# Performance work log

Measured on AMD Instinct MI355X. Metric: run time of the kernel, lower is better.

Reference implementation:

```python
import jax, jax.numpy as jnp
import numpy as np

# ---- static hyperparameters (from init_kwargs) ----
O_CH = 256        # out_channels
C_IN = 128        # in_channels
K = 3             # kernel_size
M = 9             # ALSH appended dims (m); m/(K*K)=1 extra input channel for Q
NUM_HASHES = 5
TABLE_SIZE = 2048
R = 4.0           # LSH bucket width
U = 0.99          # norm scaling constant
PAD = 1


def _conv(x, w):
    # NCHW conv, stride 1, padding 1, dilation 1 (per init_kwargs)
    return jax.lax.conv_general_dilated(
        x, w, window_strides=(1, 1), padding=[(PAD, PAD), (PAD, PAD)],
        dimension_numbers=("NCHW", "OIHW", "NCHW"))


def setup_inputs() -> dict:
    key = jax.random.key(0)
    k1, k2, k3, k4, k5 = jax.random.split(key, 5)
    x = jax.random.normal(k1, (32, C_IN, 56, 56), dtype=jnp.float32)
    weight = jax.random.normal(k2, (O_CH, C_IN, K, K), dtype=jnp.float32) * 0.05
    bias = jax.random.normal(k3, (O_CH,), dtype=jnp.float32) * 0.01
    # one stable-distribution hash vector per hash; dim = K*K*C_IN + M = 1161
    a = jax.random.normal(k4, (NUM_HASHES, K * K * C_IN + M), dtype=jnp.float32)
    b_unit = jax.random.uniform(k5, (NUM_HASHES,), dtype=jnp.float32)  # b = b_unit * R
    return {"x": x, "weight": weight, "bias": bias, "a": a, "b_unit": b_unit}


def reference(x, weight, bias, a, b_unit):
    B, C, H, W = x.shape
    O = weight.shape[0]
    b = b_unit * R  # b ~ U(0, r)

    # ---- table build: hash every kernel row (P = append norm powers) ----
    flat = weight.reshape(O, -1)                                   # [O, C*K*K]
    denom = jnp.linalg.norm(flat, axis=1).max()
    wU = (U / denom) * flat                                        # all rows ||.|| <= U < 1
    norms = jnp.linalg.norm(wU, axis=1)                            # [O]
    powers = norms[:, None] ** (2.0 ** jnp.arange(1, M + 1))       # [O, M]: ||x||^2,...,||x||^(2^M)
    Pw = jnp.concatenate([wU, powers], axis=1)                     # [O, C*K*K + M]
    hv = jnp.floor((Pw @ a.T + b[None, :]) / R).astype(jnp.int32)  # [O, NUM_HASHES]
    kernel_bucket = jnp.abs(jnp.fmod(hv, TABLE_SIZE))              # bucket of each kernel per hash

    # ---- vote: Q appends m/(K*K) channels of 0.5, conv with hash vectors as kernels ----
    extra = M // (K * K)
    xQ = jnp.concatenate(
        [x, jnp.full((B, extra, H, W), 0.5, dtype=x.dtype)], axis=1)  # [B, C+extra, H, W]
    a_kernel = a.reshape(NUM_HASHES, C + extra, K, K)
    dotted = _conv(xQ, a_kernel)                                   # [B, NUM_HASHES, H', W']
    dotted = jnp.transpose(dotted, (1, 0, 2, 3)).reshape(NUM_HASHES, -1)
    votes = jnp.floor((dotted + b[:, None]) / R).astype(jnp.int32)
    votes = jnp.abs(jnp.fmod(votes, TABLE_SIZE))                   # [NUM_HASHES, N]

    # per-hash bucket histogram via offset bincount, then best bucket per hash
    offset = (votes + jnp.arange(NUM_HASHES, dtype=jnp.int32)[:, None] * TABLE_SIZE).reshape(-1)
    counts = jnp.bincount(offset, length=NUM_HASHES * TABLE_SIZE).reshape(NUM_HASHES, TABLE_SIZE)
    selected = jnp.argmax(counts, axis=1).astype(jnp.int32)        # [NUM_HASHES]

    # ---- active set: union over selected buckets of kernels hashed there (any hash) ----
    active = jnp.any(kernel_bucket[:, :, None] == selected[None, None, :], axis=(1, 2))  # [O]
    # fallback (source draws random rows if empty): use all kernels
    active = jnp.where(jnp.any(active), active, jnp.ones_like(active))
    n_active = active.sum().astype(x.dtype)

    # ---- conv with active subset (static-shape: mask inactive output channels) ----
    out = _conv(x, weight) + bias[None, :, None, None]             # [B, O, H', W']
    out = out * active.astype(out.dtype)[None, :, None, None]
    out = out * (jnp.asarray(O, out.dtype) / n_active)             # out /= (|rows|/O)
    return out
```

## Files before the change

kernel.cpp:

```cpp
#include <hip/hip_runtime.h>
#include <hip/hip_bf16.h>
#include <stdint.h>

typedef __attribute__((ext_vector_type(8))) short  short8;
typedef __attribute__((ext_vector_type(4))) float  f32x4;

#define C_IN  128
#define O_CH  256
#define NH    5
#define TSIZE 2048
#define HWDIM 56
#define NPIX  3136
#define MTOT  100352
#define KTOT  1152
#define ADIM  1161
#define PADW  58
#define PPIX  3364
#define NHC   8
#define LBINS 192

static __device__ __forceinline__ unsigned short f2bf(float f) {
  unsigned int u = __float_as_uint(f);
  return (unsigned short)((u + 0x7fffu + ((u >> 16) & 1u)) >> 16);
}

static __device__ __forceinline__ void gload16(const unsigned short* g, unsigned short* l) {
  __builtin_amdgcn_global_load_lds(
      (const __attribute__((address_space(1))) void*)g,
      (__attribute__((address_space(3))) void*)l, 16, 0, 0);
}

#define WAITV(n) asm volatile("s_waitcnt vmcnt(" #n ")" ::: "memory")
static __device__ __forceinline__ void barsync() {
  asm volatile("" ::: "memory");
  __builtin_amdgcn_s_barrier();
  __builtin_amdgcn_sched_barrier(0);
  asm volatile("" ::: "memory");
}

__global__ void k_norms(const float* __restrict__ w, double* __restrict__ ssbuf) {
  int o = blockIdx.x, t = threadIdx.x;
  double ss = 0.;
  for (int i = t; i < KTOT; i += 64) { double v = (double)w[o * KTOT + i]; ss += v * v; }
  #pragma unroll
  for (int off = 32; off > 0; off >>= 1) ss += __shfl_down(ss, off, 64);
  if (t == 0) ssbuf[o] = ss;
}

__global__ __launch_bounds__(256) void k_table(const float* __restrict__ w,
    const float* __restrict__ a, const float* __restrict__ b_unit,
    const double* __restrict__ ssbuf, int* __restrict__ kbucket) {
  int o = blockIdx.x, t = threadIdx.x;
  __shared__ double red[256];
  __shared__ double r6[6][256];
  red[t] = ssbuf[t];
  __syncthreads();
  for (int s = 128; s; s >>= 1) { if (t < s) red[t] = fmax(red[t], red[t + s]); __syncthreads(); }
  double scale = 0.99 / sqrt(red[0]);
  double pd0 = 0, pd1 = 0, pd2 = 0, pd3 = 0, pd4 = 0, ss2 = 0;
  for (int i = t; i < KTOT; i += 256) {
    double wv = scale * (double)w[o * KTOT + i];
    ss2 += wv * wv;
    pd0 += wv * (double)a[0 * ADIM + i];
    pd1 += wv * (double)a[1 * ADIM + i];
    pd2 += wv * (double)a[2 * ADIM + i];
    pd3 += wv * (double)a[3 * ADIM + i];
    pd4 += wv * (double)a[4 * ADIM + i];
  }
  r6[0][t] = ss2; r6[1][t] = pd0; r6[2][t] = pd1; r6[3][t] = pd2; r6[4][t] = pd3; r6[5][t] = pd4;
  __syncthreads();
  for (int s = 128; s; s >>= 1) {
    if (t < s) { for (int q = 0; q < 6; ++q) r6[q][t] += r6[q][t + s]; }
    __syncthreads();
  }
  if (t == 0) {
    double nrm = sqrt(r6[0][0]);
    double q = nrm;
    double dp[NH] = {0, 0, 0, 0, 0};
    for (int j = 0; j < 9; ++j) {
      q = q * q;
      #pragma unroll
      for (int h = 0; h < NH; ++h) dp[h] += q * (double)a[h * ADIM + KTOT + j];
    }
    #pragma unroll
    for (int h = 0; h < NH; ++h) {
      double tot = r6[1 + h][0] + dp[h] + (double)b_unit[h] * 4.0;
      int hv = (int)floor(tot * 0.25);
      int bk = hv % TSIZE; if (bk < 0) bk = -bk;
      kbucket[o * NH + h] = bk;
    }
  }
}

__global__ __launch_bounds__(256) void k_prep(const float* __restrict__ w,
    const float* __restrict__ a, unsigned short* __restrict__ wpk,
    unsigned short* __restrict__ xpq, float* __restrict__ apk,
    int* __restrict__ ghist, int doPack, int qstride) {
  int bid = blockIdx.x, t = threadIdx.x;
  if (bid < 1152) {
    if (!doPack) return;
    int idx = bid * 256 + t;
    int kt = idx >> 13; int rem = idx & 8191;
    int o = rem >> 5; int cl = rem & 31;
    int kyx = kt >> 2, cq = kt & 3;
    wpk[idx] = f2bf(w[o * KTOT + (cq * 32 + cl) * 9 + kyx]);
  } else if (bid < 1175) {
    int i = (bid - 1152) * 256 + t;
    if (i < C_IN * 45) {
      int c = i / 45, r = i - c * 45;
      int h = r / 9, k = r - h * 9;
      apk[c * 48 + r] = a[h * ADIM + c * 9 + k];
    }
  } else if (bid < 1215) {
    int i = (bid - 1175) * 2048 + t;
    #pragma unroll
    for (int j = 0; j < 8; ++j) ghist[i + j * 256] = 0;
  } else {
    if (!doPack) return;
    int b2 = bid - 1215;
    int cq = b2 & 3; int rest = b2 >> 2;
    int r = rest % PADW, bl = rest / PADW;
    unsigned short* row = xpq + ((size_t)cq * qstride + (size_t)bl * PPIX + (size_t)r * PADW) * 32;
    if (r == 0 || r == PADW - 1) {
      for (int i = t; i < PADW * 32; i += 256) row[i] = 0;
    } else {
      if (t < 32) row[t] = 0;
      else if (t < 64) row[57 * 32 + (t - 32)] = 0;
    }
  }
}

__global__ __launch_bounds__(256) void k_vote3a(const float* __restrict__ x,
    const float* __restrict__ apk, float* __restrict__ pdot) {
  int g = blockIdx.y;
  int t = threadIdx.x;
  int p0 = blockIdx.x * 512 + t * 2;
  int bb = p0 / NPIX; int rem = p0 - bb * NPIX;
  int y = rem / HWDIM; int xxL = rem - y * HWDIM;
  bool xm = xxL > 0, xp = xxL < HWDIM - 2;
  bool y0 = y > 0, y2 = y < HWDIM - 1;
  const float* xb = x + ((size_t)bb * C_IN + g * 32) * NPIX + y * HWDIM + xxL;
  const float* ap = apk + (g * 32) * 48;
  float aL[NH] = {0, 0, 0, 0, 0}, aR[NH] = {0, 0, 0, 0, 0};
  for (int c = 0; c < 32; ++c) {
    const float* xc = xb + c * NPIX;
    float t0m = 0, t00 = 0, t01 = 0, t02 = 0;
    float m0m = 0, m02 = 0;
    float b0m = 0, b00 = 0, b01 = 0, b02 = 0;
    float m00 = xc[0], m01 = xc[1];
    if (xm) m0m = xc[-1];
    if (xp) m02 = xc[2];
    if (y0) { t00 = xc[-HWDIM]; t01 = xc[-HWDIM + 1]; if (xm) t0m = xc[-HWDIM - 1]; if (xp) t02 = xc[-HWDIM + 2]; }
    if (y2) { b00 = xc[HWDIM];  b01 = xc[HWDIM + 1];  if (xm) b0m = xc[HWDIM - 1];  if (xp) b02 = xc[HWDIM + 2]; }
    const float* ac = ap + c * 48;
    #pragma unroll
    for (int h = 0; h < NH; ++h) {
      const float* ah = ac + h * 9;
      aL[h] += t0m * ah[0] + t00 * ah[1] + t01 * ah[2] + m0m * ah[3] + m00 * ah[4]
             + m01 * ah[5] + b0m * ah[6] + b00 * ah[7] + b01 * ah[8];
      aR[h] += t00 * ah[0] + t01 * ah[1] + t02 * ah[2] + m00 * ah[3] + m01 * ah[4]
             + m02 * ah[5] + b00 * ah[6] + b01 * ah[7] + b02 * ah[8];
    }
  }
  #pragma unroll
  for (int h = 0; h < NH; ++h) {
    float2 v = make_float2(aL[h], aR[h]);
    *(float2*)&pdot[((size_t)g * NH + h) * MTOT + p0] = v;
  }
}

__global__ __launch_bounds__(256) void k_vote3b(const float* __restrict__ pdot,
    const float* __restrict__ a, const float* __restrict__ b_unit, int* __restrict__ ghist) {
  __shared__ int lh[NH * LBINS];
  int t = threadIdx.x;
  for (int i = t; i < NH * LBINS; i += 256) lh[i] = 0;
  __syncthreads();
  int p = blockIdx.x * 256 + t;
  int bb = p / NPIX; int rem = p - bb * NPIX;
  int y = rem / HWDIM; int xx = rem - y * HWDIM;
  bool x0 = xx > 0, x2 = xx < HWDIM - 1, y0 = y > 0, y2 = y < HWDIM - 1;
  int* gh = ghist + (blockIdx.x & (NHC - 1)) * NH * TSIZE;
  #pragma unroll
  for (int h = 0; h < NH; ++h) {
    float s = pdot[((size_t)0 * NH + h) * MTOT + p] + pdot[((size_t)1 * NH + h) * MTOT + p]
            + pdot[((size_t)2 * NH + h) * MTOT + p] + pdot[((size_t)3 * NH + h) * MTOT + p];
    const float* ah = a + h * ADIM + KTOT;
    float e = ah[4];
    if (x0) e += ah[3];
    if (x2) e += ah[5];
    if (y0) { e += ah[1]; if (x0) e += ah[0]; if (x2) e += ah[2]; }
    if (y2) { e += ah[7]; if (x0) e += ah[6]; if (x2) e += ah[8]; }
    s += 0.5f * e;
    int hv = (int)floorf((s + b_unit[h] * 4.0f) * 0.25f);
    int bk = hv % TSIZE; if (bk < 0) bk = -bk;
    if (bk < LBINS) atomicAdd(&lh[h * LBINS + bk], 1);
    else            atomicAdd(&gh[h * TSIZE + bk], 1);
  }
  __syncthreads();
  for (int i = t; i < NH * LBINS; i += 256) {
    int v = lh[i];
    if (v) { int h = i / LBINS, bk = i - h * LBINS; atomicAdd(&gh[h * TSIZE + bk], v); }
  }
}

__global__ __launch_bounds__(256) void k_vote2(const float* __restrict__ x,
    const float* __restrict__ a, const float* __restrict__ b_unit, int* __restrict__ ghist) {
  __shared__ float red[4][NH][64];
  __shared__ int   lh[NH * LBINS];
  int t = threadIdx.x;
  int px = t & 63, g = t >> 6;
  for (int i = t; i < NH * LBINS; i += 256) lh[i] = 0;
  int p = blockIdx.x * 64 + px;
  int bb = p / NPIX; int rem = p - bb * NPIX;
  int y = rem / HWDIM; int xx = rem - y * HWDIM;
  bool x0 = xx > 0, x2 = xx < HWDIM - 1, y0 = y > 0, y2 = y < HWDIM - 1;
  const float* xb = x + ((size_t)bb * C_IN + g * 32) * NPIX + y * HWDIM + xx;
  float acc[NH] = {0, 0, 0, 0, 0};
  for (int c = 0; c < 32; ++c) {
    const float* xc = xb + c * NPIX;
    float v0 = 0, v1 = 0, v2 = 0, v3 = 0, v5 = 0, v6 = 0, v7 = 0, v8 = 0;
    float v4 = xc[0];
    if (x0) v3 = xc[-1];
    if (x2) v5 = xc[1];
    if (y0) { v1 = xc[-HWDIM]; if (x0) v0 = xc[-HWDIM - 1]; if (x2) v2 = xc[-HWDIM + 1]; }
    if (y2) { v7 = xc[HWDIM];  if (x0) v6 = xc[HWDIM - 1];  if (x2) v8 = xc[HWDIM + 1]; }
    #pragma unroll
    for (int h = 0; h < NH; ++h) {
      const float* ah = a + h * ADIM + (g * 32 + c) * 9;
      acc[h] += v0 * ah[0] + v1 * ah[1] + v2 * ah[2] + v3 * ah[3] + v4 * ah[4]
              + v5 * ah[5] + v6 * ah[6] + v7 * ah[7] + v8 * ah[8];
    }
  }
  #pragma unroll
  for (int h = 0; h < NH; ++h) red[g][h][px] = acc[h];
  __syncthreads();
  int* gh = ghist + (blockIdx.x & (NHC - 1)) * NH * TSIZE;
  if (g == 0) {
    #pragma unroll
    for (int h = 0; h < NH; ++h) {
      float s = red[0][h][px] + red[1][h][px] + red[2][h][px] + red[3][h][px];
      const float* ah = a + h * ADIM + KTOT;
      float e = ah[4];
      if (x0) e += ah[3];
      if (x2) e += ah[5];
      if (y0) { e += ah[1]; if (x0) e += ah[0]; if (x2) e += ah[2]; }
      if (y2) { e += ah[7]; if (x0) e += ah[6]; if (x2) e += ah[8]; }
      s += 0.5f * e;
      int hv = (int)floorf((s + b_unit[h] * 4.0f) * 0.25f);
      int bk = hv % TSIZE; if (bk < 0) bk = -bk;
      if (bk < LBINS) atomicAdd(&lh[h * LBINS + bk], 1);
      else            atomicAdd(&gh[h * TSIZE + bk], 1);
    }
  }
  __syncthreads();
  for (int i = t; i < NH * LBINS; i += 256) {
    int v = lh[i];
    if (v) { int h = i / LBINS, bk = i - h * LBINS; atomicAdd(&gh[h * TSIZE + bk], v); }
  }
}

__global__ __launch_bounds__(256) void k_argmax(const int* __restrict__ ghist, int* __restrict__ sel) {
  int h = blockIdx.x;
  int t = threadIdx.x;
  __shared__ int rc[256], ri[256];
  int bc = -1, bi = 0;
  for (int i = t; i < TSIZE; i += 256) {
    int c = 0;
    #pragma unroll
    for (int k = 0; k < NHC; ++k) c += ghist[(k * NH + h) * TSIZE + i];
    if (c > bc) { bc = c; bi = i; }
  }
  rc[t] = bc; ri[t] = bi;
  __syncthreads();
  for (int s = 128; s; s >>= 1) {
    if (t < s) {
      if (rc[t + s] > rc[t] || (rc[t + s] == rc[t] && ri[t + s] < ri[t])) {
        rc[t] = rc[t + s]; ri[t] = ri[t + s];
      }
    }
    __syncthreads();
  }
  if (t == 0) sel[h] = ri[0];
}

__global__ __launch_bounds__(256) void k_mask(const int* __restrict__ sel,
    const int* __restrict__ kbucket, float* __restrict__ mscale) {
  int t = threadIdx.x;
  __shared__ int cnt[256], ssel[NH];
  if (t < NH) ssel[t] = sel[t];
  __syncthreads();
  bool act = false;
  #pragma unroll
  for (int i = 0; i < NH; ++i) {
    int kb = kbucket[t * NH + i];
    #pragma unroll
    for (int j = 0; j < NH; ++j) act = act || (kb == ssel[j]);
  }
  cnt[t] = act ? 1 : 0;
  __syncthreads();
  for (int s = 128; s; s >>= 1) { if (t < s) cnt[t] += cnt[t + s]; __syncthreads(); }
  int n = cnt[0];
  bool a2 = act;
  if (n == 0) { a2 = true; n = 256; }
  mscale[t] = a2 ? 256.0f / (float)n : 0.0f;
}

__global__ __launch_bounds__(256) void k_packx1(const float* __restrict__ x, int b0,
                                                unsigned short* __restrict__ xpq, int qstride) {
  int bl = blockIdx.x / HWDIM; int y = blockIdx.x - bl * HWDIM;
  int t = threadIdx.x;
  __shared__ unsigned short th[C_IN * 57];
  const float* xb = x + (size_t)((b0 + bl) * C_IN) * NPIX + y * HWDIM;
  for (int i = t; i < C_IN * HWDIM; i += 256) {
    int c = i / HWDIM; int xx = i - c * HWDIM;
    th[c * 57 + xx] = f2bf(xb[c * NPIX + xx]);
  }
  __syncthreads();
  size_t pbase = (size_t)bl * PPIX + (size_t)(y + 1) * PADW + 1;
  for (int i = t; i < C_IN * HWDIM; i += 256) {
    int xx = i >> 7; int c = i & 127;
    xpq[((size_t)(c >> 5) * qstride + pbase + xx) * 32 + (c & 31)] = th[c * 57 + xx];
  }
}

__global__ __launch_bounds__(256, 4) void k_gemmA(
    const unsigned short* __restrict__ xpq, const unsigned short* __restrict__ wpk,
    const float* __restrict__ bias, const float* __restrict__ mscale,
    float* __restrict__ out, int b0, int qstride) {
  int nwg = gridDim.x, orig = blockIdx.x;
  int q = nwg >> 3, r = nwg & 7, xcd = orig & 7, loc = orig >> 3;
  int bid = (xcd < r ? xcd * (q + 1) : r * (q + 1) + (xcd - r) * q) + loc;
  int mtile = bid >> 1;
  int ntile = bid & 1;
  int tid = threadIdx.x;
  int lane = tid & 63, wv = tid >> 6;
  int wr = wv >> 1, wc = wv & 1;
  __shared__ __attribute__((aligned(16))) unsigned short As[2][128 * 32];
  __shared__ __attribute__((aligned(16))) unsigned short Bs[2][128 * 32];

  int r0 = tid >> 2;
  int sst = (r0 & 3) ^ ((r0 >> 2) & 3);
  int che8 = ((tid & 3) ^ sst) << 3;
  int pixA0, pixA1;
  {
    int mg = mtile * 128 + r0;
    int bb = (unsigned)mg / NPIX; int rem = mg - bb * NPIX;
    int y = (unsigned)rem / HWDIM; int xx = rem - y * HWDIM;
    pixA0 = bb * PPIX + y * PADW + xx;
    mg = mtile * 128 + 64 + r0;
    bb = (unsigned)mg / NPIX; rem = mg - bb * NPIX;
    y = (unsigned)rem / HWDIM; xx = rem - y * HWDIM;
    pixA1 = bb * PPIX + y * PADW + xx;
  }
  int srcB0 = (ntile * 128 + r0) * 32 + che8;
  int srcB1 = (ntile * 128 + 64 + r0) * 32 + che8;
  int dst0 = (tid & 192) * 8;
  int dst1 = 2048 + dst0;

  f32x4 acc[4][4];
  #pragma unroll
  for (int mi = 0; mi < 4; ++mi)
    #pragma unroll
    for (int ni = 0; ni < 4; ++ni) acc[mi][ni] = (f32x4){0.f, 0.f, 0.f, 0.f};

  int ar = lane & 15, hi = lane >> 4;
  int sr = (ar & 3) ^ ((ar >> 2) & 3);
  int rdc = (hi ^ sr) << 3;

  gload16(xpq + (size_t)pixA0 * 32 + che8, &As[0][dst0]);
  gload16(xpq + (size_t)pixA1 * 32 + che8, &As[0][dst1]);
  gload16(wpk + srcB0, &Bs[0][dst0]);
  gload16(wpk + srcB1, &Bs[0][dst1]);

  for (int kt = 0; kt < 36; ++kt) {
    int buf = kt & 1;
    if (kt < 35) {
      int st = kt + 1, sb = st & 1, stap = st >> 2;
      int ky = stap / 3, kx = stap - ky * 3;
      size_t qoff = (size_t)(st & 3) * qstride + (ky * PADW + kx);
      gload16(xpq + (qoff + pixA0) * 32 + che8, &As[sb][dst0]);
      gload16(xpq + (qoff + pixA1) * 32 + che8, &As[sb][dst1]);
      gload16(wpk + st * 8192 + srcB0, &Bs[sb][dst0]);
      gload16(wpk + st * 8192 + srcB1, &Bs[sb][dst1]);
      WAITV(4);
    } else {
      WAITV(0);
    }
    barsync();
    short8 af[4], bf[4];
    #pragma unroll
    for (int mi = 0; mi < 4; ++mi) af[mi] = *(const short8*)&As[buf][(wr * 64 + mi * 16 + ar) * 32 + rdc];
    #pragma unroll
    for (int ni = 0; ni < 4; ++ni) bf[ni] = *(const short8*)&Bs[buf][(wc * 64 + ni * 16 + ar) * 32 + rdc];
    #pragma unroll
    for (int mi = 0; mi < 4; ++mi)
      #pragma unroll
      for (int ni = 0; ni < 4; ++ni)
        acc[mi][ni] = __builtin_amdgcn_mfma_f32_16x16x32_bf16(af[mi], bf[ni], acc[mi][ni], 0, 0, 0);
    barsync();
  }

  int r4 = hi << 2;
  int cn = ar;
  #pragma unroll
  for (int ni = 0; ni < 4; ++ni) {
    int o = ntile * 128 + wc * 64 + ni * 16 + cn;
    float ms = mscale[o], bi = bias[o];
    #pragma unroll
    for (int mi = 0; mi < 4; ++mi) {
      int mg = mtile * 128 + wr * 64 + mi * 16 + r4;
      int bb = (unsigned)mg / NPIX; int pix = mg - bb * NPIX;
      f32x4 v;
      #pragma unroll
      for (int j = 0; j < 4; ++j) v[j] = (acc[mi][ni][j] + bi) * ms;
      *(f32x4*)(out + (size_t)(((b0 + bb) << 8) + o) * NPIX + pix) = v;
    }
  }
}

__global__ __launch_bounds__(256) void k_dconv(const float* __restrict__ x,
    const float* __restrict__ w, const float* __restrict__ bias,
    const float* __restrict__ mscale, float* __restrict__ out) {
  int bid = blockIdx.x;
  int yq = bid % 14; int rem = bid / 14;
  int o = rem & 255; int b = rem >> 8;
  __shared__ float wsm[KTOT];
  for (int i = threadIdx.x; i < KTOT; i += 256) wsm[i] = w[o * KTOT + i];
  __syncthreads();
  int t = threadIdx.x;
  if (t >= 224) return;
  int y = yq * 4 + t / HWDIM;
  int xx = t % HWDIM;
  const float* xb = x + (size_t)b * C_IN * NPIX + y * HWDIM + xx;
  float acc = 0.f;
  bool y0 = y > 0, y2 = y < HWDIM - 1, x0 = xx > 0, x2 = xx < HWDIM - 1;
  for (int c = 0; c < C_IN; ++c) {
    const float* xc = xb + c * NPIX;
    const float* wc9 = wsm + c * 9;
    float s = xc[0] * wc9[4];
    if (x0) s += xc[-1] * wc9[3];
    if (x2) s += xc[1] * wc9[5];
    if (y0) { s += xc[-HWDIM] * wc9[1]; if (x0) s += xc[-HWDIM - 1] * wc9[0]; if (x2) s += xc[-HWDIM + 1] * wc9[2]; }
    if (y2) { s += xc[HWDIM] * wc9[7];  if (x0) s += xc[HWDIM - 1] * wc9[6];  if (x2) s += xc[HWDIM + 1] * wc9[8]; }
    acc += s;
  }
  out[((size_t)b * O_CH + o) * NPIX + y * HWDIM + xx] = (acc + bias[o]) * mscale[o];
}

extern "C" void kernel_launch(void* const* d_in, const int* in_sizes, int n_in,
                              void* d_out, int out_size, void* d_ws, size_t ws_size,
                              hipStream_t stream) {
  const float* x      = (const float*)d_in[0];
  const float* w      = (const float*)d_in[1];
  const float* bias   = (const float*)d_in[2];
  const float* a      = (const float*)d_in[3];
  const float* b_unit = (const float*)d_in[4];
  float* out = (float*)d_out;
  char* ws = (char*)d_ws;

  int*    ghist   = (int*)   (ws);
  double* ssbuf   = (double*)(ws + 327680);
  int*    kbucket = (int*)   (ws + 329728);
  float*  mscale  = (float*) (ws + 334848);
  float*  apk     = (float*) (ws + 335872);
  int*    sel     = (int*)   (ws + 360448);
  const size_t SMALL = 360512;
  const size_t PDOT  = 8028160;
  float* pdot = (float*)(ws + SMALL);

  bool twopass = ws_size >= SMALL + PDOT;
  const size_t GBASE = SMALL + (twopass ? PDOT : 0);
  const size_t WPT = 589824;
  const size_t XPB = 861184;
  int NB = 0;
  for (int nb = 32; nb >= 2; nb -= 2)
    if (GBASE + WPT + (size_t)nb * XPB <= ws_size) { NB = nb; break; }
  int qstride = NB * PPIX;

  unsigned short* wpk = (unsigned short*)(ws + GBASE);
  unsigned short* xpq = (unsigned short*)(ws + GBASE + WPT);

  k_prep<<<1215 + NB * PADW * 4, 256, 0, stream>>>(w, a, wpk, xpq, apk, ghist,
                                                   NB > 0 ? 1 : 0, qstride);

  k_norms <<<256, 64, 0, stream>>>(w, ssbuf);
  k_table <<<256, 256, 0, stream>>>(w, a, b_unit, ssbuf, kbucket);

  if (twopass) {
    k_vote3a<<<dim3(196, 4), 256, 0, stream>>>(x, apk, pdot);
    k_vote3b<<<392, 256, 0, stream>>>(pdot, a, b_unit, ghist);
  } else {
    k_vote2 <<<1568, 256, 0, stream>>>(x, a, b_unit, ghist);
  }
  k_argmax<<<NH, 256, 0, stream>>>(ghist, sel);
  k_mask  <<<1, 256, 0, stream>>>(sel, kbucket, mscale);

  if (NB == 0) {
    k_dconv<<<32 * 256 * 14, 256, 0, stream>>>(x, w, bias, mscale, out);
    return;
  }

  for (int b0 = 0; b0 < 32; b0 += NB) {
    int nb = NB < (32 - b0) ? NB : (32 - b0);
    k_packx1<<<nb * HWDIM, 256, 0, stream>>>(x, b0, xpq, qstride);
    int mtiles = nb * NPIX / 128;
    k_gemmA<<<mtiles * 2, 256, 0, stream>>>(xpq, wpk, bias, mscale, out, b0, qstride);
  }
}
```

Before: 171.3 us.

## Widen GEMM tile to full 256 output channels with 512-thread blocks

The implicit-GEMM conv kernel now has each 512-thread workgroup compute a 128-pixel by 256-channel tile instead of splitting channels across two 256-thread workgroups. Each activation tile is loaded from global memory once instead of twice, and grid size is halved. The trade-offs are a larger shared-memory footprint per block (B buffer doubled) and possibly lower occupancy, since the launch bound no longer requests multiple blocks per CU.

```diff
diff --git a/kernel.cpp b/kernel.cpp
--- a/kernel.cpp
+++ b/kernel.cpp
@@ -323,39 +323,34 @@
   }
 }
 
-__global__ __launch_bounds__(256, 4) void k_gemmA(
+__global__ __launch_bounds__(512) void k_gemmB(
     const unsigned short* __restrict__ xpq, const unsigned short* __restrict__ wpk,
     const float* __restrict__ bias, const float* __restrict__ mscale,
     float* __restrict__ out, int b0, int qstride) {
   int nwg = gridDim.x, orig = blockIdx.x;
   int q = nwg >> 3, r = nwg & 7, xcd = orig & 7, loc = orig >> 3;
-  int bid = (xcd < r ? xcd * (q + 1) : r * (q + 1) + (xcd - r) * q) + loc;
-  int mtile = bid >> 1;
-  int ntile = bid & 1;
+  int mtile = (xcd < r ? xcd * (q + 1) : r * (q + 1) + (xcd - r) * q) + loc;
   int tid = threadIdx.x;
-  int lane = tid & 63, wv = tid >> 6;
-  int wr = wv >> 1, wc = wv & 1;
+  int lane = tid & 63, wid = tid >> 6;
+  int wm = wid >> 2, wn = wid & 3;
   __shared__ __attribute__((aligned(16))) unsigned short As[2][128 * 32];
-  __shared__ __attribute__((aligned(16))) unsigned short Bs[2][128 * 32];
+  __shared__ __attribute__((aligned(16))) unsigned short Bs[2][256 * 32];
 
   int r0 = tid >> 2;
   int sst = (r0 & 3) ^ ((r0 >> 2) & 3);
   int che8 = ((tid & 3) ^ sst) << 3;
-  int pixA0, pixA1;
+  int pixA;
   {
     int mg = mtile * 128 + r0;
     int bb = (unsigned)mg / NPIX; int rem = mg - bb * NPIX;
     int y = (unsigned)rem / HWDIM; int xx = rem - y * HWDIM;
-    pixA0 = bb * PPIX + y * PADW + xx;
-    mg = mtile * 128 + 64 + r0;
-    bb = (unsigned)mg / NPIX; rem = mg - bb * NPIX;
-    y = (unsigned)rem / HWDIM; xx = rem - y * HWDIM;
-    pixA1 = bb * PPIX + y * PADW + xx;
-  }
-  int srcB0 = (ntile * 128 + r0) * 32 + che8;
-  int srcB1 = (ntile * 128 + 64 + r0) * 32 + che8;
-  int dst0 = (tid & 192) * 8;
-  int dst1 = 2048 + dst0;
+    pixA = bb * PPIX + y * PADW + xx;
+  }
+  int srcB0 = r0 * 32 + che8;
+  int srcB1 = (128 + r0) * 32 + che8;
+  int dstA  = (tid & 448) * 8;
+  int dstB0 = dstA;
+  int dstB1 = 4096 + dstA;
 
   f32x4 acc[4][4];
   #pragma unroll
@@ -367,10 +362,9 @@
   int sr = (ar & 3) ^ ((ar >> 2) & 3);
   int rdc = (hi ^ sr) << 3;
 
-  gload16(xpq + (size_t)pixA0 * 32 + che8, &As[0][dst0]);
-  gload16(xpq + (size_t)pixA1 * 32 + che8, &As[0][dst1]);
-  gload16(wpk + srcB0, &Bs[0][dst0]);
-  gload16(wpk + srcB1, &Bs[0][dst1]);
+  gload16(xpq + (size_t)pixA * 32 + che8, &As[0][dstA]);
+  gload16(wpk + srcB0, &Bs[0][dstB0]);
+  gload16(wpk + srcB1, &Bs[0][dstB1]);
 
   for (int kt = 0; kt < 36; ++kt) {
     int buf = kt & 1;
@@ -378,20 +372,19 @@
       int st = kt + 1, sb = st & 1, stap = st >> 2;
       int ky = stap / 3, kx = stap - ky * 3;
       size_t qoff = (size_t)(st & 3) * qstride + (ky * PADW + kx);
-      gload16(xpq + (qoff + pixA0) * 32 + che8, &As[sb][dst0]);
-      gload16(xpq + (qoff + pixA1) * 32 + che8, &As[sb][dst1]);
-      gload16(wpk + st * 8192 + srcB0, &Bs[sb][dst0]);
-      gload16(wpk + st * 8192 + srcB1, &Bs[sb][dst1]);
-      WAITV(4);
+      gload16(xpq + (qoff + pixA) * 32 + che8, &As[sb][dstA]);
+      gload16(wpk + st * 8192 + srcB0, &Bs[sb][dstB0]);
+      gload16(wpk + st * 8192 + srcB1, &Bs[sb][dstB1]);
+      WAITV(3);
     } else {
       WAITV(0);
     }
     barsync();
     short8 af[4], bf[4];
     #pragma unroll
-    for (int mi = 0; mi < 4; ++mi) af[mi] = *(const short8*)&As[buf][(wr * 64 + mi * 16 + ar) * 32 + rdc];
-    #pragma unroll
-    for (int ni = 0; ni < 4; ++ni) bf[ni] = *(const short8*)&Bs[buf][(wc * 64 + ni * 16 + ar) * 32 + rdc];
+    for (int mi = 0; mi < 4; ++mi) af[mi] = *(const short8*)&As[buf][(wm * 64 + mi * 16 + ar) * 32 + rdc];
+    #pragma unroll
+    for (int ni = 0; ni < 4; ++ni) bf[ni] = *(const short8*)&Bs[buf][(wn * 64 + ni * 16 + ar) * 32 + rdc];
     #pragma unroll
     for (int mi = 0; mi < 4; ++mi)
       #pragma unroll
@@ -404,11 +397,11 @@
   int cn = ar;
   #pragma unroll
   for (int ni = 0; ni < 4; ++ni) {
-    int o = ntile * 128 + wc * 64 + ni * 16 + cn;
+    int o = wn * 64 + ni * 16 + cn;
     float ms = mscale[o], bi = bias[o];
     #pragma unroll
     for (int mi = 0; mi < 4; ++mi) {
-      int mg = mtile * 128 + wr * 64 + mi * 16 + r4;
+      int mg = mtile * 128 + wm * 64 + mi * 16 + r4;
       int bb = (unsigned)mg / NPIX; int pix = mg - bb * NPIX;
       f32x4 v;
       #pragma unroll
@@ -504,6 +497,6 @@
     int nb = NB < (32 - b0) ? NB : (32 - b0);
     k_packx1<<<nb * HWDIM, 256, 0, stream>>>(x, b0, xpq, qstride);
     int mtiles = nb * NPIX / 128;
-    k_gemmA<<<mtiles * 2, 256, 0, stream>>>(xpq, wpk, bias, mscale, out, b0, qstride);
-  }
-}
+    k_gemmB<<<mtiles, 512, 0, stream>>>(xpq, wpk, bias, mscale, out, b0, qstride);
+  }
+}
```

Result: slower. 178.7 us (+4.3%).
